# Kernel optimization log

Hardware: AMD Instinct MI355X
Metric: run time of the kernel (lower is better)

Reference implementation:

```python
import jax, jax.numpy as jnp
import numpy as np

B, TE, U, IN_DIM = 128, 2048, 256, 256  # batch, encoder_ts, units(=encoder_latdim), input_dim


def setup_inputs() -> dict:
    key = jax.random.key(0)
    ks = jax.random.split(key, 16)
    s = 0.05
    return {
        "inputs": jax.random.normal(ks[0], (B, IN_DIM), jnp.float32),
        "h_tm": jax.random.normal(ks[1], (B, U), jnp.float32),
        "x_seq": jax.random.normal(ks[2], (B, TE, U), jnp.float32),
        "V_a": jax.random.normal(ks[3], (U,), jnp.float32) * s,
        "W_a": jax.random.normal(ks[4], (U, U), jnp.float32) * s,
        "U_a": jax.random.normal(ks[5], (U, U), jnp.float32) * s,
        "b_a": jnp.zeros((U,), jnp.float32),
        "C_z": jax.random.normal(ks[6], (IN_DIM + U, U), jnp.float32) * s,
        "W_z": jax.random.normal(ks[7], (U, U), jnp.float32) * s,
        "b_z": jnp.zeros((U,), jnp.float32),
        "C_r": jax.random.normal(ks[8], (IN_DIM + U, U), jnp.float32) * s,
        "W_r": jax.random.normal(ks[9], (U, U), jnp.float32) * s,
        "b_r": jnp.zeros((U,), jnp.float32),
        "C_p": jax.random.normal(ks[10], (IN_DIM + U, U), jnp.float32) * s,
        "U_p": jax.random.normal(ks[11], (U, U), jnp.float32) * s,
        "b_p": jnp.zeros((U,), jnp.float32),
    }


def reference(inputs, h_tm, x_seq, V_a, W_a, U_a, b_a,
              C_z, W_z, b_z, C_r, W_r, b_r, C_p, U_p, b_p):
    # Additive attention over encoder timesteps.
    uxpb = jnp.einsum("bte,eu->btu", x_seq, U_a) + b_a          # [B,TE,U]
    wxstm = h_tm @ W_a                                            # [B,U]
    et = jnp.einsum("btu,u->bt", jnp.tanh(wxstm[:, None, :] + uxpb), V_a)  # [B,TE]
    # Original uses unnormalized exp / sum (no max-subtraction)
    at = jnp.exp(et)
    at = at / jnp.sum(at, axis=1, keepdims=True)                  # [B,TE]
    context = jnp.einsum("bt,bte->be", at, x_seq)                 # [B,U]
    ci = jnp.concatenate([inputs, context], axis=1)               # [B,IN+U]
    zt = jax.nn.sigmoid(h_tm @ W_z + ci @ C_z + b_z)
    rt = jax.nn.sigmoid(h_tm @ W_r + ci @ C_r + b_r)
    t_ht = jnp.tanh((rt * h_tm) @ U_p + ci @ C_p + b_p)
    ht = (1.0 - zt) * h_tm + zt * t_ht
    return ht
```

## Files before the change

### kernel.cpp

```cpp
#include <hip/hip_runtime.h>

#define BB 128
#define TE 2048
#define UU 256
#define IN_DIM 256
#define MC 32
#define NCH 8
#define GPB 8

typedef float f32x4 __attribute__((ext_vector_type(4)));
typedef __fp16 f16x2 __attribute__((ext_vector_type(2)));
typedef _Float16 f16x8 __attribute__((ext_vector_type(8)));

__device__ __forceinline__ float fast_tanh(float x) {
  float e = __expf(2.f * x);
  return 1.f - 2.f / (e + 1.f);
}
__device__ __forceinline__ float fast_sigmoid(float x) {
  return 1.f / (1.f + __expf(-x));
}
__device__ __forceinline__ void bar_lds() {
  asm volatile("s_waitcnt lgkmcnt(0)" ::: "memory");
  __builtin_amdgcn_s_barrier();
}

__global__ __launch_bounds__(256) void prep_kernel(
    const float* __restrict__ h_tm, const float* __restrict__ W_a,
    const float* __restrict__ b_a, const float* __restrict__ U_a,
    float* __restrict__ addvec, _Float16* __restrict__ UhT2) {
  int t = threadIdx.x;
  if (blockIdx.x < BB) {
    int bi = blockIdx.x;
    __shared__ float hL[UU];
    hL[t] = h_tm[bi * UU + t];
    __syncthreads();
    float s = b_a[t];
    for (int e = 0; e < UU; ++e) s += hL[e] * W_a[e * UU + t];
    addvec[bi * UU + t] = s;
  } else {
    int b2 = blockIdx.x - BB;
    int n = t;
    union { f16x8 v; _Float16 h[8]; } pk;
#pragma unroll
    for (int e = 0; e < 8; ++e) pk.h[e] = (_Float16)U_a[(b2 * 8 + e) * UU + n];
    *(f16x8*)(UhT2 + ((b2 * UU + n) << 3)) = pk.v;
  }
}

__global__ __launch_bounds__(256, 2) void attn_main(
    const float* __restrict__ x_seq, const float* __restrict__ V_a,
    const _Float16* __restrict__ UhT2, const float* __restrict__ addvec,
    float* __restrict__ numw, float* __restrict__ denw) {
  __shared__ __align__(16) float Xb[2][MC * UU];
  __shared__ float avL[UU], vaL[UU];
  __shared__ float wsum[4][MC];
  __shared__ float eL[MC];

  const int tid = threadIdx.x;
  const int bi = blockIdx.x >> 3;
  const int g = blockIdx.x & 7;
  const float* xc = x_seq + (size_t)(bi * TE + g * (MC * NCH)) * UU;

  const int w = tid >> 6, l = tid & 63, lr = l & 15, lg = l >> 4;
  const int rlow = lr & 7;

  f32x4 st[8];
#pragma unroll
  for (int j = 0; j < 8; ++j) st[j] = *(const f32x4*)(xc + (size_t)(j * 256 + tid) * 4);

  avL[tid] = addvec[bi * UU + tid];
  vaL[tid] = V_a[tid];

  f16x8 Bf[8][4];
#pragma unroll
  for (int ks = 0; ks < 8; ++ks)
#pragma unroll
    for (int ni = 0; ni < 4; ++ni) {
      int n = w * 64 + ni * 16 + lr;
      Bf[ks][ni] = *(const f16x8*)(UhT2 + (((ks * 4 + lg) * UU + n) << 3));
    }

  {
    float* B0 = &Xb[0][0];
#pragma unroll
    for (int j = 0; j < 8; ++j) {
      int row = j * 4 + (tid >> 6), u = tid & 63;
      *(f32x4*)(B0 + (((row << 6) + (u ^ (row & 7))) << 2)) = st[j];
    }
  }
#pragma unroll
  for (int j = 0; j < 8; ++j)
    st[j] = *(const f32x4*)(xc + (size_t)(MC * UU) + (size_t)(j * 256 + tid) * 4);
  bar_lds();

  float num_acc = 0.f, den_acc = 0.f;
  for (int i = 0; i < NCH; ++i) {
    const float* Xc = &Xb[i & 1][0];
    f32x4 acc[2][4];
#pragma unroll
    for (int mi = 0; mi < 2; ++mi)
#pragma unroll
      for (int ni = 0; ni < 4; ++ni) acc[mi][ni] = (f32x4)0.f;

#pragma unroll
    for (int ks = 0; ks < 8; ++ks) {
      f16x8 a[2];
#pragma unroll
      for (int mi = 0; mi < 2; ++mi) {
        const int rowoff = (mi * 16 + lr) << 8;
        int u0 = ks * 8 + lg * 2;
        f32x4 f0 = *(const f32x4*)(Xc + rowoff + ((u0 ^ rlow) << 2));
        f32x4 f1 = *(const f32x4*)(Xc + rowoff + (((u0 + 1) ^ rlow) << 2));
        union { f16x8 v; f16x2 p[4]; } A;
        A.p[0] = __builtin_amdgcn_cvt_pkrtz(f0.x, f0.y);
        A.p[1] = __builtin_amdgcn_cvt_pkrtz(f0.z, f0.w);
        A.p[2] = __builtin_amdgcn_cvt_pkrtz(f1.x, f1.y);
        A.p[3] = __builtin_amdgcn_cvt_pkrtz(f1.z, f1.w);
        a[mi] = A.v;
      }
#pragma unroll
      for (int mi = 0; mi < 2; ++mi)
#pragma unroll
        for (int ni = 0; ni < 4; ++ni)
          acc[mi][ni] = __builtin_amdgcn_mfma_f32_16x16x32_f16(a[mi], Bf[ks][ni],
                                                               acc[mi][ni], 0, 0, 0);
    }

    float psum[2][4];
#pragma unroll
    for (int mi = 0; mi < 2; ++mi)
#pragma unroll
      for (int r = 0; r < 4; ++r) psum[mi][r] = 0.f;
#pragma unroll
    for (int ni = 0; ni < 4; ++ni) {
      int n = w * 64 + ni * 16 + lr;
      float av = avL[n], va = vaL[n];
#pragma unroll
      for (int mi = 0; mi < 2; ++mi)
#pragma unroll
        for (int r = 0; r < 4; ++r)
          psum[mi][r] += fast_tanh(acc[mi][ni][r] + av) * va;
    }
#pragma unroll
    for (int off = 1; off < 16; off <<= 1)
#pragma unroll
      for (int mi = 0; mi < 2; ++mi)
#pragma unroll
        for (int r = 0; r < 4; ++r) psum[mi][r] += __shfl_xor(psum[mi][r], off, 64);
    if (lr == 0) {
#pragma unroll
      for (int mi = 0; mi < 2; ++mi)
#pragma unroll
        for (int r = 0; r < 4; ++r) wsum[w][mi * 16 + lg * 4 + r] = psum[mi][r];
    }
    bar_lds();
    if (tid < MC) {
      float et = wsum[0][tid] + wsum[1][tid] + wsum[2][tid] + wsum[3][tid];
      eL[tid] = __expf(et);
    }
    bar_lds();

#pragma unroll 8
    for (int m = 0; m < MC; ++m) {
      float e = eL[m];
      num_acc += e * Xc[(m << 8) + ((((tid >> 2) ^ (m & 7))) << 2) + (tid & 3)];
      den_acc += e;
    }

    if (i < NCH - 1) {
      float* Bn = &Xb[(i + 1) & 1][0];
#pragma unroll
      for (int j = 0; j < 8; ++j) {
        int row = j * 4 + (tid >> 6), u = tid & 63;
        *(f32x4*)(Bn + (((row << 6) + (u ^ (row & 7))) << 2)) = st[j];
      }
      if (i < NCH - 2) {
        const float* src = xc + (size_t)(i + 2) * (MC * UU);
#pragma unroll
        for (int j = 0; j < 8; ++j) st[j] = *(const f32x4*)(src + (size_t)(j * 256 + tid) * 4);
      }
      bar_lds();
    }
  }
  numw[(bi * GPB + g) * UU + tid] = num_acc;
  if (tid == 0) denw[bi * GPB + g] = den_acc;
}

__global__ __launch_bounds__(1024) void finalize_kernel(
    const float* __restrict__ inputs, const float* __restrict__ h_tm,
    const float* __restrict__ numw, const float* __restrict__ denw,
    const float* __restrict__ C_z, const float* __restrict__ W_z,
    const float* __restrict__ b_z, const float* __restrict__ C_r,
    const float* __restrict__ W_r, const float* __restrict__ b_r,
    const float* __restrict__ C_p, const float* __restrict__ U_p,
    const float* __restrict__ b_p, float* __restrict__ out) {
  int bi = blockIdx.x, tid = threadIdx.x;
  int t = tid & 255, s = tid >> 8;
  __shared__ float hL[UU], ciL[IN_DIM + UU], rhL[UU];
  __shared__ float zp[4][UU], rp[4][UU], pp[4][UU];

  if (s == 0) {
    float ns = 0.f;
#pragma unroll
    for (int c = 0; c < GPB; ++c) ns += numw[(bi * GPB + c) * UU + t];
    float ds = 0.f;
#pragma unroll
    for (int c = 0; c < GPB; ++c) ds += denw[bi * GPB + c];
    ciL[IN_DIM + t] = ns / ds;
    ciL[t] = inputs[bi * IN_DIM + t];
    hL[t] = h_tm[bi * UU + t];
  }
  __syncthreads();

  float z = 0.f, r = 0.f, p = 0.f;
  for (int e = s * 64; e < s * 64 + 64; ++e) {
    float h = hL[e];
    z += h * W_z[e * UU + t];
    r += h * W_r[e * UU + t];
  }
  for (int e = s * 128; e < s * 128 + 128; ++e) {
    float cv = ciL[e];
    z += cv * C_z[e * UU + t];
    r += cv * C_r[e * UU + t];
    p += cv * C_p[e * UU + t];
  }
  zp[s][t] = z; rp[s][t] = r; pp[s][t] = p;
  __syncthreads();

  if (s == 0) {
    float zz = zp[0][t] + zp[1][t] + zp[2][t] + zp[3][t] + b_z[t];
    float rr = rp[0][t] + rp[1][t] + rp[2][t] + rp[3][t] + b_r[t];
    zz = fast_sigmoid(zz);
    rr = fast_sigmoid(rr);
    zp[0][t] = zz;
    rhL[t] = rr * hL[t];
  }
  __syncthreads();

  float p2 = 0.f;
  for (int e = s * 64; e < s * 64 + 64; ++e) p2 += rhL[e] * U_p[e * UU + t];
  pp[s][t] += p2;
  __syncthreads();

  if (s == 0) {
    float pt = pp[0][t] + pp[1][t] + pp[2][t] + pp[3][t] + b_p[t];
    float th = fast_tanh(pt);
    float zz = zp[0][t];
    out[bi * UU + t] = (1.f - zz) * hL[t] + zz * th;
  }
}

extern "C" void kernel_launch(void* const* d_in, const int* in_sizes, int n_in,
                              void* d_out, int out_size, void* d_ws, size_t ws_size,
                              hipStream_t stream) {
  const float* inputs = (const float*)d_in[0];
  const float* h_tm = (const float*)d_in[1];
  const float* x_seq = (const float*)d_in[2];
  const float* V_a = (const float*)d_in[3];
  const float* W_a = (const float*)d_in[4];
  const float* U_a = (const float*)d_in[5];
  const float* b_a = (const float*)d_in[6];
  const float* C_z = (const float*)d_in[7];
  const float* W_z = (const float*)d_in[8];
  const float* b_z = (const float*)d_in[9];
  const float* C_r = (const float*)d_in[10];
  const float* W_r = (const float*)d_in[11];
  const float* b_r = (const float*)d_in[12];
  const float* C_p = (const float*)d_in[13];
  const float* U_p = (const float*)d_in[14];
  const float* b_p = (const float*)d_in[15];

  _Float16* UhT2 = (_Float16*)d_ws;
  float* addvec = (float*)((char*)d_ws + 131072);
  float* numw = (float*)((char*)d_ws + 262144);
  float* denw = (float*)((char*)d_ws + 262144 + 1048576);
  float* out = (float*)d_out;

  prep_kernel<<<BB + 32, 256, 0, stream>>>(h_tm, W_a, b_a, U_a, addvec, UhT2);
  attn_main<<<BB * GPB, 256, 0, stream>>>(x_seq, V_a, UhT2, addvec, numw, denw);
  finalize_kernel<<<BB, 1024, 0, stream>>>(inputs, h_tm, numw, denw, C_z, W_z, b_z,
                                           C_r, W_r, b_r, C_p, U_p, b_p, out);
}
```

Baseline: 564.2 us.

## Stage x chunks as fp16 in LDS, reload B fragments per k-step, simplify finalize

The attention kernel now converts each x_seq chunk to fp16 once, when it is written to LDS, instead of converting on every MFMA operand read. This halves LDS usage and removes repeated conversions. The U_a fragments are loaded from global/L2 inside each k-step rather than held in 128 registers, which frees registers so the launch bound can rise to 4 blocks per CU. The risks are that the weighted context sum now reads fp16-rounded x values, and that more B-fragment memory traffic lands inside the loop. The finalize kernel drops from 1024 to 256 threads and removes the partial-sum reductions, which gives each thread a longer serial dot product.

```diff
diff --git a/kernel.cpp b/kernel.cpp
--- a/kernel.cpp
+++ b/kernel.cpp
@@ -47,11 +47,11 @@
   }
 }
 
-__global__ __launch_bounds__(256, 2) void attn_main(
+__global__ __launch_bounds__(256, 4) void attn_main(
     const float* __restrict__ x_seq, const float* __restrict__ V_a,
     const _Float16* __restrict__ UhT2, const float* __restrict__ addvec,
     float* __restrict__ numw, float* __restrict__ denw) {
-  __shared__ __align__(16) float Xb[2][MC * UU];
+  __shared__ __align__(16) _Float16 Xh[2][MC * UU];
   __shared__ float avL[UU], vaL[UU];
   __shared__ float wsum[4][MC];
   __shared__ float eL[MC];
@@ -62,7 +62,6 @@
   const float* xc = x_seq + (size_t)(bi * TE + g * (MC * NCH)) * UU;
 
   const int w = tid >> 6, l = tid & 63, lr = l & 15, lg = l >> 4;
-  const int rlow = lr & 7;
 
   f32x4 st[8];
 #pragma unroll
@@ -71,21 +70,15 @@
   avL[tid] = addvec[bi * UU + tid];
   vaL[tid] = V_a[tid];
 
-  f16x8 Bf[8][4];
-#pragma unroll
-  for (int ks = 0; ks < 8; ++ks)
-#pragma unroll
-    for (int ni = 0; ni < 4; ++ni) {
-      int n = w * 64 + ni * 16 + lr;
-      Bf[ks][ni] = *(const f16x8*)(UhT2 + (((ks * 4 + lg) * UU + n) << 3));
-    }
-
   {
-    float* B0 = &Xb[0][0];
+    _Float16* B0 = &Xh[0][0];
 #pragma unroll
     for (int j = 0; j < 8; ++j) {
-      int row = j * 4 + (tid >> 6), u = tid & 63;
-      *(f32x4*)(B0 + (((row << 6) + (u ^ (row & 7))) << 2)) = st[j];
+      int row = j * 4 + w;
+      union { unsigned long long u; f16x2 p[2]; } pk;
+      pk.p[0] = __builtin_amdgcn_cvt_pkrtz(st[j].x, st[j].y);
+      pk.p[1] = __builtin_amdgcn_cvt_pkrtz(st[j].z, st[j].w);
+      *(unsigned long long*)(B0 + (row << 8) + ((l * 4) ^ ((row & 7) << 3))) = pk.u;
     }
   }
 #pragma unroll
@@ -95,7 +88,7 @@
 
   float num_acc = 0.f, den_acc = 0.f;
   for (int i = 0; i < NCH; ++i) {
-    const float* Xc = &Xb[i & 1][0];
+    const _Float16* Xc = &Xh[i & 1][0];
     f32x4 acc[2][4];
 #pragma unroll
     for (int mi = 0; mi < 2; ++mi)
@@ -104,25 +97,24 @@
 
 #pragma unroll
     for (int ks = 0; ks < 8; ++ks) {
+      f16x8 Bf[4];
+#pragma unroll
+      for (int ni = 0; ni < 4; ++ni) {
+        int n = w * 64 + ni * 16 + lr;
+        Bf[ni] = *(const f16x8*)(UhT2 + (((ks * 4 + lg) * UU + n) << 3));
+      }
       f16x8 a[2];
 #pragma unroll
       for (int mi = 0; mi < 2; ++mi) {
-        const int rowoff = (mi * 16 + lr) << 8;
-        int u0 = ks * 8 + lg * 2;
-        f32x4 f0 = *(const f32x4*)(Xc + rowoff + ((u0 ^ rlow) << 2));
-        f32x4 f1 = *(const f32x4*)(Xc + rowoff + (((u0 + 1) ^ rlow) << 2));
-        union { f16x8 v; f16x2 p[4]; } A;
-        A.p[0] = __builtin_amdgcn_cvt_pkrtz(f0.x, f0.y);
-        A.p[1] = __builtin_amdgcn_cvt_pkrtz(f0.z, f0.w);
-        A.p[2] = __builtin_amdgcn_cvt_pkrtz(f1.x, f1.y);
-        A.p[3] = __builtin_amdgcn_cvt_pkrtz(f1.z, f1.w);
-        a[mi] = A.v;
+        int row = mi * 16 + lr;
+        a[mi] = *(const f16x8*)(Xc + (row << 8) +
+                                ((ks * 32 + lg * 8) ^ ((row & 7) << 3)));
       }
 #pragma unroll
       for (int mi = 0; mi < 2; ++mi)
 #pragma unroll
         for (int ni = 0; ni < 4; ++ni)
-          acc[mi][ni] = __builtin_amdgcn_mfma_f32_16x16x32_f16(a[mi], Bf[ks][ni],
+          acc[mi][ni] = __builtin_amdgcn_mfma_f32_16x16x32_f16(a[mi], Bf[ni],
                                                                acc[mi][ni], 0, 0, 0);
     }
 
@@ -163,16 +155,19 @@
 #pragma unroll 8
     for (int m = 0; m < MC; ++m) {
       float e = eL[m];
-      num_acc += e * Xc[(m << 8) + ((((tid >> 2) ^ (m & 7))) << 2) + (tid & 3)];
+      num_acc += e * (float)Xc[(m << 8) + (tid ^ ((m & 7) << 3))];
       den_acc += e;
     }
 
     if (i < NCH - 1) {
-      float* Bn = &Xb[(i + 1) & 1][0];
+      _Float16* Bn = &Xh[(i + 1) & 1][0];
 #pragma unroll
       for (int j = 0; j < 8; ++j) {
-        int row = j * 4 + (tid >> 6), u = tid & 63;
-        *(f32x4*)(Bn + (((row << 6) + (u ^ (row & 7))) << 2)) = st[j];
+        int row = j * 4 + w;
+        union { unsigned long long u; f16x2 p[2]; } pk;
+        pk.p[0] = __builtin_amdgcn_cvt_pkrtz(st[j].x, st[j].y);
+        pk.p[1] = __builtin_amdgcn_cvt_pkrtz(st[j].z, st[j].w);
+        *(unsigned long long*)(Bn + (row << 8) + ((l * 4) ^ ((row & 7) << 3))) = pk.u;
       }
       if (i < NCH - 2) {
         const float* src = xc + (size_t)(i + 2) * (MC * UU);
@@ -186,7 +181,7 @@
   if (tid == 0) denw[bi * GPB + g] = den_acc;
 }
 
-__global__ __launch_bounds__(1024) void finalize_kernel(
+__global__ __launch_bounds__(256) void finalize_kernel(
     const float* __restrict__ inputs, const float* __restrict__ h_tm,
     const float* __restrict__ numw, const float* __restrict__ denw,
     const float* __restrict__ C_z, const float* __restrict__ W_z,
@@ -194,60 +189,38 @@
     const float* __restrict__ W_r, const float* __restrict__ b_r,
     const float* __restrict__ C_p, const float* __restrict__ U_p,
     const float* __restrict__ b_p, float* __restrict__ out) {
-  int bi = blockIdx.x, tid = threadIdx.x;
-  int t = tid & 255, s = tid >> 8;
+  int bi = blockIdx.x, t = threadIdx.x;
   __shared__ float hL[UU], ciL[IN_DIM + UU], rhL[UU];
-  __shared__ float zp[4][UU], rp[4][UU], pp[4][UU];
-
-  if (s == 0) {
-    float ns = 0.f;
-#pragma unroll
-    for (int c = 0; c < GPB; ++c) ns += numw[(bi * GPB + c) * UU + t];
-    float ds = 0.f;
-#pragma unroll
-    for (int c = 0; c < GPB; ++c) ds += denw[bi * GPB + c];
-    ciL[IN_DIM + t] = ns / ds;
-    ciL[t] = inputs[bi * IN_DIM + t];
-    hL[t] = h_tm[bi * UU + t];
-  }
+  float ns = 0.f;
+#pragma unroll
+  for (int c = 0; c < GPB; ++c) ns += numw[(bi * GPB + c) * UU + t];
+  float ds = 0.f;
+#pragma unroll
+  for (int c = 0; c < GPB; ++c) ds += denw[bi * GPB + c];
+  ciL[IN_DIM + t] = ns / ds;
+  ciL[t] = inputs[bi * IN_DIM + t];
+  hL[t] = h_tm[bi * UU + t];
   __syncthreads();
 
-  float z = 0.f, r = 0.f, p = 0.f;
-  for (int e = s * 64; e < s * 64 + 64; ++e) {
+  float z = b_z[t], r = b_r[t], p = b_p[t];
+  for (int e = 0; e < UU; ++e) {
     float h = hL[e];
     z += h * W_z[e * UU + t];
     r += h * W_r[e * UU + t];
   }
-  for (int e = s * 128; e < s * 128 + 128; ++e) {
+  for (int e = 0; e < IN_DIM + UU; ++e) {
     float cv = ciL[e];
     z += cv * C_z[e * UU + t];
     r += cv * C_r[e * UU + t];
     p += cv * C_p[e * UU + t];
   }
-  zp[s][t] = z; rp[s][t] = r; pp[s][t] = p;
+  z = fast_sigmoid(z);
+  r = fast_sigmoid(r);
+  rhL[t] = r * hL[t];
   __syncthreads();
-
-  if (s == 0) {
-    float zz = zp[0][t] + zp[1][t] + zp[2][t] + zp[3][t] + b_z[t];
-    float rr = rp[0][t] + rp[1][t] + rp[2][t] + rp[3][t] + b_r[t];
-    zz = fast_sigmoid(zz);
-    rr = fast_sigmoid(rr);
-    zp[0][t] = zz;
-    rhL[t] = rr * hL[t];
-  }
-  __syncthreads();
-
-  float p2 = 0.f;
-  for (int e = s * 64; e < s * 64 + 64; ++e) p2 += rhL[e] * U_p[e * UU + t];
-  pp[s][t] += p2;
-  __syncthreads();
-
-  if (s == 0) {
-    float pt = pp[0][t] + pp[1][t] + pp[2][t] + pp[3][t] + b_p[t];
-    float th = fast_tanh(pt);
-    float zz = zp[0][t];
-    out[bi * UU + t] = (1.f - zz) * hL[t] + zz * th;
-  }
+  for (int e = 0; e < UU; ++e) p += rhL[e] * U_p[e * UU + t];
+  float th = fast_tanh(p);
+  out[bi * UU + t] = (1.f - z) * hL[t] + z * th;
 }
 
 extern "C" void kernel_launch(void* const* d_in, const int* in_sizes, int n_in,
@@ -278,6 +251,6 @@
 
   prep_kernel<<<BB + 32, 256, 0, stream>>>(h_tm, W_a, b_a, U_a, addvec, UhT2);
   attn_main<<<BB * GPB, 256, 0, stream>>>(x_seq, V_a, UhT2, addvec, numw, denw);
-  finalize_kernel<<<BB, 1024, 0, stream>>>(inputs, h_tm, numw, denw, C_z, W_z, b_z,
-                                           C_r, W_r, b_r, C_p, U_p, b_p, out);
-}
+  finalize_kernel<<<BB, 256, 0, stream>>>(inputs, h_tm, numw, denw, C_z, W_z, b_z,
+                                          C_r, W_r, b_r, C_p, U_p, b_p, out);
+}
```

Result: slower. 684.3 us (+21.3%).
